# Kernel tuning notes

Measured on AMD Instinct MI355X. Metric: run time of the kernel, lower is better.

The kernel has to match this reference:

```python
import jax, jax.numpy as jnp
import numpy as np

N_NODES = 10000
EPS = 1e-5


def _layernorm(x, gamma, beta):
    mu = jnp.mean(x, axis=-1, keepdims=True)
    var = jnp.mean(jnp.square(x - mu), axis=-1, keepdims=True)
    return (x - mu) * jax.lax.rsqrt(var + EPS) * gamma + beta


def _sage_pool_layer(h, src, dst, Wp, bp, Ws, Wn, b, gamma, beta):
    # DGL SAGEConv(aggregator='pool'):
    #   m_u = relu(h_u @ Wp^T + bp); h_neigh[v] = max_{u in N(v)} m_u (0 if no neighbors)
    #   rst = h @ Ws^T + h_neigh @ Wn^T + b
    m = jax.nn.relu(h @ Wp.T + bp)              # [N, d]
    msg = m[src]                                 # [E, d] gather
    agg = jax.ops.segment_max(msg, dst, num_segments=N_NODES)
    agg = jnp.where(jnp.isfinite(agg), agg, 0.0)  # isolated nodes -> 0
    rst = h @ Ws.T + agg @ Wn.T + b
    # gsage_layer: LayerNorm, then Encoder applies relu (dropout inactive in eval)
    return jax.nn.relu(_layernorm(rst, gamma, beta))


def setup_inputs() -> dict:
    key = jax.random.key(0)
    ks = jax.random.split(key, 16)
    d = 256
    E = 320000
    s = 1.0 / np.sqrt(d)
    inp = {
        "h": jax.random.normal(ks[0], (N_NODES, d), dtype=jnp.float32),
        "edge_src": jax.random.randint(ks[1], (E,), 0, N_NODES, dtype=jnp.int32),
        "edge_dst": jax.random.randint(ks[2], (E,), 0, N_NODES, dtype=jnp.int32),
    }
    for li in range(2):
        kk = jax.random.split(ks[3 + li], 3)
        inp[f"Wp{li}"] = jax.random.normal(kk[0], (d, d), dtype=jnp.float32) * s
        inp[f"bp{li}"] = jnp.zeros((d,), jnp.float32)
        inp[f"Ws{li}"] = jax.random.normal(kk[1], (d, d), dtype=jnp.float32) * s
        inp[f"Wn{li}"] = jax.random.normal(kk[2], (d, d), dtype=jnp.float32) * s
        inp[f"b{li}"] = jnp.zeros((d,), jnp.float32)
        inp[f"g{li}"] = jnp.ones((d,), jnp.float32)
        inp[f"be{li}"] = jnp.zeros((d,), jnp.float32)
    return inp


def reference(h, edge_src, edge_dst,
              Wp0, bp0, Ws0, Wn0, b0, g0, be0,
              Wp1, bp1, Ws1, Wn1, b1, g1, be1):
    h = _sage_pool_layer(h, edge_src, edge_dst, Wp0, bp0, Ws0, Wn0, b0, g0, be0)
    h = _sage_pool_layer(h, edge_src, edge_dst, Wp1, bp1, Ws1, Wn1, b1, g1, be1)
    return h
```

## Files before the change

kernel.cpp:

```cpp
#include <hip/hip_runtime.h>

#define D 256
#define CAP 128
#define ASTRIDE 280
#define LN_EPS 1e-5f

typedef short short8 __attribute__((ext_vector_type(8)));
typedef float floatx4 __attribute__((ext_vector_type(4)));
typedef unsigned short u16x4 __attribute__((ext_vector_type(4)));

typedef const __attribute__((address_space(1))) void* gas_t;
typedef __attribute__((address_space(3))) void* las_t;

#define WAIT_VM(n) __builtin_amdgcn_s_waitcnt(((n) & 0xF) | (((n) >> 4) << 14) | (7 << 4) | (0xF << 8))

__device__ __forceinline__ u16x4 umax4(u16x4 a, u16x4 b) {
#if __has_builtin(__builtin_elementwise_max)
    return __builtin_elementwise_max(a, b);
#else
    u16x4 r;
    r.x = a.x > b.x ? a.x : b.x; r.y = a.y > b.y ? a.y : b.y;
    r.z = a.z > b.z ? a.z : b.z; r.w = a.w > b.w ? a.w : b.w;
    return r;
#endif
}

__device__ __forceinline__ unsigned short f2b(float f) {
    union { float f; unsigned int u; } x; x.f = f;
    unsigned int u = x.u + 0x7FFFu + ((x.u >> 16) & 1u);
    return (unsigned short)(u >> 16);
}

#define GEMM_HALF(APTR_EXPR, WPTR, K0H)                                         \
    {                                                                           \
        short8 aF[4], bF[4][4];                                                 \
        _Pragma("unroll") for (int ks = 0; ks < 4; ks++)                        \
            aF[ks] = APTR_EXPR(K0H + ks * 32);                                  \
        _Pragma("unroll") for (int ks = 0; ks < 4; ks++)                        \
        _Pragma("unroll") for (int t = 0; t < 4; t++)                           \
            bF[ks][t] = *(const short8*)((WPTR) + t * 16 * D + (K0H) + ks * 32);\
        _Pragma("unroll") for (int ks = 0; ks < 4; ks++) {                      \
            acc[0] = __builtin_amdgcn_mfma_f32_16x16x32_bf16(aF[ks], bF[ks][0], acc[0], 0, 0, 0); \
            acc[1] = __builtin_amdgcn_mfma_f32_16x16x32_bf16(aF[ks], bF[ks][1], acc[1], 0, 0, 0); \
            acc[2] = __builtin_amdgcn_mfma_f32_16x16x32_bf16(aF[ks], bF[ks][2], acc[2], 0, 0, 0); \
            acc[3] = __builtin_amdgcn_mfma_f32_16x16x32_bf16(aF[ks], bF[ks][3], acc[3], 0, 0, 0); \
        }                                                                       \
    }

__global__ __launch_bounds__(256) void prep_kernel(
    const float* __restrict__ w0, const float* __restrict__ w1,
    const float* __restrict__ w2, const float* __restrict__ w3,
    const float* __restrict__ w4, const float* __restrict__ w5,
    unsigned short* __restrict__ wb,
    const float* __restrict__ h, unsigned short* __restrict__ hb, int nh4,
    int* __restrict__ cnt, unsigned short* __restrict__ mb, int N)
{
    const int blk = blockIdx.x;
    const int tid = threadIdx.x;
    if (blk < 384) {
        const int wsel = blk >> 6;
        const float* src;
        switch (wsel) {
            case 0: src = w0; break; case 1: src = w1; break;
            case 2: src = w2; break; case 3: src = w3; break;
            case 4: src = w4; break; default: src = w5; break;
        }
        const int idx = (blk & 63) * 1024 + tid * 4;
        const float4 v = *(const float4*)(src + idx);
        ushort4 o;
        o.x = f2b(v.x); o.y = f2b(v.y); o.z = f2b(v.z); o.w = f2b(v.w);
        *(ushort4*)(wb + (size_t)wsel * 65536 + idx) = o;
    } else if (blk < 1024) {
        int i = (blk - 384) * 256 + tid;
        const int stride = 640 * 256;
        for (; i < nh4; i += stride) {
            const float4 v = *(const float4*)(h + (size_t)i * 4);
            ushort4 o;
            o.x = f2b(v.x); o.y = f2b(v.y); o.z = f2b(v.z); o.w = f2b(v.w);
            *(ushort4*)(hb + (size_t)i * 4) = o;
        }
    } else if (blk < 1064) {
        const int i = (blk - 1024) * 256 + tid;
        if (i < N) cnt[i] = 0;
    } else {
        mb[(size_t)N * D + tid] = 0;
    }
}

__global__ __launch_bounds__(64, 4) void gemm_relu(
    const unsigned short* __restrict__ A, const unsigned short* __restrict__ W,
    const float* __restrict__ bias, unsigned short* __restrict__ out_b, int N,
    const int* __restrict__ esrc, const int* __restrict__ edst,
    int* __restrict__ cnt, unsigned short* __restrict__ csr, int E, int ngemm)
{
    if ((int)blockIdx.x >= ngemm) {
        const int nsb = gridDim.x - ngemm;
        int i = ((int)blockIdx.x - ngemm) * 64 + threadIdx.x;
        const int stride = nsb * 64;
        for (; i < E; i += stride) {
            const int d = edst[i];
            const int pos = atomicAdd(&cnt[d], 1);
            if (pos < CAP) csr[(size_t)d * CAP + pos] = (unsigned short)esrc[i];
        }
        return;
    }

    const int lane = threadIdx.x;
    const int quad = lane >> 4;
    const int l16 = lane & 15;
    const int blk = blockIdx.x;
    const int row0 = (blk >> 2) * 16;
    const int col0 = (blk & 3) * 64;
    const int koff = quad * 8;

    floatx4 acc[4];
#pragma unroll
    for (int t = 0; t < 4; t++) acc[t] = (floatx4)(0.f);

    const unsigned short* aptr = A + (size_t)(row0 + l16) * D + koff;
    const unsigned short* wptr = W + (size_t)(col0 + l16) * D + koff;
#define A_GLOBAL(K) (*(const short8*)(aptr + (K)))
    GEMM_HALF(A_GLOBAL, wptr, 0)
    GEMM_HALF(A_GLOBAL, wptr, 128)
#undef A_GLOBAL

#pragma unroll
    for (int t = 0; t < 4; t++) {
        const float bcol = bias[col0 + t * 16 + l16];
#pragma unroll
        for (int r = 0; r < 4; r++) {
            const int rg = row0 + quad * 4 + r;
            const int col = col0 + t * 16 + l16;
            out_b[(size_t)rg * D + col] = f2b(fmaxf(acc[t][r] + bcol, 0.f));
        }
    }
}

__global__ __launch_bounds__(256, 3) void gemm_ln_pool(
    const unsigned short* __restrict__ A, const unsigned short* __restrict__ Wself,
    const unsigned short* __restrict__ Wneigh,
    const unsigned short* __restrict__ mpool,
    const int* __restrict__ cnt, const unsigned short* __restrict__ csr,
    const float* __restrict__ bias,
    const float* __restrict__ gamma, const float* __restrict__ beta,
    unsigned short* __restrict__ out_b, float* __restrict__ out_f,
    const unsigned short* __restrict__ Wnext, const float* __restrict__ bnext,
    unsigned short* __restrict__ mout, int N)
{
    __shared__ unsigned short idxS[16][CAP];
    __shared__ unsigned short gbuf[4][2][8][D];
    __shared__ unsigned short aggS[16 * ASTRIDE];
    __shared__ float redS[4][16], redS2[4][16], muA[16], rsA[16];

    const int tid = threadIdx.x;
    const int wave = tid >> 6;
    const int lane = tid & 63;
    const int quad = lane >> 4;
    const int l16 = lane & 15;
    const int row0 = blockIdx.x * 16;
    const int koff = quad * 8;
    const int rbase = wave * 4;
    const int half = lane >> 5;
    const int l32 = lane & 31;

    int degs[4];
#pragma unroll
    for (int rr = 0; rr < 4; rr++) degs[rr] = min(cnt[row0 + rbase + rr], CAP);
    int P = max(max(degs[0], degs[1]), max(degs[2], degs[3]));
    const int P2 = (P + 1) & ~1;
#pragma unroll
    for (int rr = 0; rr < 4; rr++) {
        const int rg = row0 + rbase + rr;
        for (int i = lane; i < P2; i += 64)
            idxS[rbase + rr][i] = (i < degs[rr]) ? csr[(size_t)rg * CAP + i]
                                                 : (unsigned short)N;
    }

    floatx4 acc[4];
#pragma unroll
    for (int t = 0; t < 4; t++) acc[t] = (floatx4)(0.f);

    {
        const unsigned short* aptr = A + (size_t)(row0 + l16) * D + koff;
        const unsigned short* wptr = Wself + (size_t)(wave * 64 + l16) * D + koff;
#pragma unroll
        for (int k0 = 0; k0 < D; k0 += 32) {
            const short8 av = *(const short8*)(aptr + k0);
            const short8 b0 = *(const short8*)(wptr + k0);
            const short8 b1 = *(const short8*)(wptr + 16 * D + k0);
            const short8 b2 = *(const short8*)(wptr + 32 * D + k0);
            const short8 b3 = *(const short8*)(wptr + 48 * D + k0);
            acc[0] = __builtin_amdgcn_mfma_f32_16x16x32_bf16(av, b0, acc[0], 0, 0, 0);
            acc[1] = __builtin_amdgcn_mfma_f32_16x16x32_bf16(av, b1, acc[1], 0, 0, 0);
            acc[2] = __builtin_amdgcn_mfma_f32_16x16x32_bf16(av, b2, acc[2], 0, 0, 0);
            acc[3] = __builtin_amdgcn_mfma_f32_16x16x32_bf16(av, b3, acc[3], 0, 0, 0);
        }
    }

    {
        const int nb = P2 >> 1;
        u16x4 mx[4];
#pragma unroll
        for (int rr = 0; rr < 4; rr++) mx[rr] = (u16x4)(0);

#define ISSUE_BURST(bi, buf)                                                    \
        {                                                                       \
            _Pragma("unroll") for (int rr = 0; rr < 4; rr++) {                  \
                const int jj = idxS[rbase + rr][2 * (bi) + half];               \
                const unsigned short* gp = mpool + (size_t)jj * D + l32 * 8;    \
                __builtin_amdgcn_global_load_lds(                               \
                    (gas_t)gp, (las_t)&gbuf[wave][buf][rr * 2][0], 16, 0, 0);   \
            }                                                                   \
        }

        if (nb > 0) ISSUE_BURST(0, 0);
        if (nb > 1) ISSUE_BURST(1, 1);
        for (int b = 0; b < nb; b++) {
            if (b + 1 < nb) WAIT_VM(4); else WAIT_VM(0);
            const int buf = b & 1;
#pragma unroll
            for (int rr = 0; rr < 4; rr++) {
                const u16x4 a0 = *(const u16x4*)&gbuf[wave][buf][rr * 2 + 0][lane * 4];
                const u16x4 a1 = *(const u16x4*)&gbuf[wave][buf][rr * 2 + 1][lane * 4];
                mx[rr] = umax4(mx[rr], umax4(a0, a1));
            }
            if (b + 2 < nb) ISSUE_BURST(b + 2, buf);
        }
#undef ISSUE_BURST
#pragma unroll
        for (int rr = 0; rr < 4; rr++)
            *(u16x4*)&aggS[(rbase + rr) * ASTRIDE + lane * 4] = mx[rr];
    }
    __syncthreads();

    {
        const unsigned short* wptr = Wneigh + (size_t)(wave * 64 + l16) * D + koff;
#pragma unroll
        for (int k0 = 0; k0 < D; k0 += 32) {
            const short8 av = *(const short8*)&aggS[l16 * ASTRIDE + koff + k0];
            const short8 b0 = *(const short8*)(wptr + k0);
            const short8 b1 = *(const short8*)(wptr + 16 * D + k0);
            const short8 b2 = *(const short8*)(wptr + 32 * D + k0);
            const short8 b3 = *(const short8*)(wptr + 48 * D + k0);
            acc[0] = __builtin_amdgcn_mfma_f32_16x16x32_bf16(av, b0, acc[0], 0, 0, 0);
            acc[1] = __builtin_amdgcn_mfma_f32_16x16x32_bf16(av, b1, acc[1], 0, 0, 0);
            acc[2] = __builtin_amdgcn_mfma_f32_16x16x32_bf16(av, b2, acc[2], 0, 0, 0);
            acc[3] = __builtin_amdgcn_mfma_f32_16x16x32_bf16(av, b3, acc[3], 0, 0, 0);
        }
    }

    float bcol[4];
#pragma unroll
    for (int t = 0; t < 4; t++) bcol[t] = bias[wave * 64 + t * 16 + l16];
#pragma unroll
    for (int t = 0; t < 4; t++)
#pragma unroll
        for (int r = 0; r < 4; r++) acc[t][r] += bcol[t];

#pragma unroll
    for (int r = 0; r < 4; r++) {
        float s = 0.f, s2 = 0.f;
#pragma unroll
        for (int t = 0; t < 4; t++) {
            const float v = acc[t][r];
            s += v; s2 += v * v;
        }
        s += __shfl_xor(s, 1);  s2 += __shfl_xor(s2, 1);
        s += __shfl_xor(s, 2);  s2 += __shfl_xor(s2, 2);
        s += __shfl_xor(s, 4);  s2 += __shfl_xor(s2, 4);
        s += __shfl_xor(s, 8);  s2 += __shfl_xor(s2, 8);
        if (l16 == 0) {
            redS[wave][quad * 4 + r] = s;
            redS2[wave][quad * 4 + r] = s2;
        }
    }
    __syncthreads();
    if (tid < 16) {
        const float S  = redS[0][tid] + redS[1][tid] + redS[2][tid] + redS[3][tid];
        const float S2 = redS2[0][tid] + redS2[1][tid] + redS2[2][tid] + redS2[3][tid];
        const float mu = S * (1.f / D);
        float var = S2 * (1.f / D) - mu * mu;
        var = fmaxf(var, 0.f);
        muA[tid] = mu;
        rsA[tid] = rsqrtf(var + LN_EPS);
    }
    __syncthreads();

    float gcol[4], becol[4];
#pragma unroll
    for (int t = 0; t < 4; t++) {
        gcol[t] = gamma[wave * 64 + t * 16 + l16];
        becol[t] = beta[wave * 64 + t * 16 + l16];
    }
#pragma unroll
    for (int r = 0; r < 4; r++) {
        const int rl = quad * 4 + r;
        const int rg = row0 + rl;
        const float mu = muA[rl];
        const float rs = rsA[rl];
#pragma unroll
        for (int t = 0; t < 4; t++) {
            const int col = wave * 64 + t * 16 + l16;
            float o = (acc[t][r] - mu) * rs * gcol[t] + becol[t];
            o = fmaxf(o, 0.f);
            const unsigned short ob = f2b(o);
            if (out_f) out_f[(size_t)rg * D + col] = o;
            else       out_b[(size_t)rg * D + col] = ob;
            if (Wnext) aggS[rl * ASTRIDE + col] = ob;
        }
    }

    if (Wnext) {
        __syncthreads();
#pragma unroll
        for (int t = 0; t < 4; t++) acc[t] = (floatx4)(0.f);
        const unsigned short* wptr = Wnext + (size_t)(wave * 64 + l16) * D + koff;
#pragma unroll
        for (int k0 = 0; k0 < D; k0 += 32) {
            const short8 av = *(const short8*)&aggS[l16 * ASTRIDE + koff + k0];
            const short8 b0 = *(const short8*)(wptr + k0);
            const short8 b1 = *(const short8*)(wptr + 16 * D + k0);
            const short8 b2 = *(const short8*)(wptr + 32 * D + k0);
            const short8 b3 = *(const short8*)(wptr + 48 * D + k0);
            acc[0] = __builtin_amdgcn_mfma_f32_16x16x32_bf16(av, b0, acc[0], 0, 0, 0);
            acc[1] = __builtin_amdgcn_mfma_f32_16x16x32_bf16(av, b1, acc[1], 0, 0, 0);
            acc[2] = __builtin_amdgcn_mfma_f32_16x16x32_bf16(av, b2, acc[2], 0, 0, 0);
            acc[3] = __builtin_amdgcn_mfma_f32_16x16x32_bf16(av, b3, acc[3], 0, 0, 0);
        }
#pragma unroll
        for (int t = 0; t < 4; t++) {
            const float bc = bnext[wave * 64 + t * 16 + l16];
#pragma unroll
            for (int r = 0; r < 4; r++) {
                const int rg = row0 + quad * 4 + r;
                const int col = wave * 64 + t * 16 + l16;
                mout[(size_t)rg * D + col] = f2b(fmaxf(acc[t][r] + bc, 0.f));
            }
        }
    }
}

extern "C" void kernel_launch(void* const* d_in, const int* in_sizes, int n_in,
                              void* d_out, int out_size, void* d_ws, size_t ws_size,
                              hipStream_t stream) {
    const float* h    = (const float*)d_in[0];
    const int*   esrc = (const int*)d_in[1];
    const int*   edst = (const int*)d_in[2];
    const float* Wp0  = (const float*)d_in[3];
    const float* bp0  = (const float*)d_in[4];
    const float* Ws0  = (const float*)d_in[5];
    const float* Wn0  = (const float*)d_in[6];
    const float* b0   = (const float*)d_in[7];
    const float* g0   = (const float*)d_in[8];
    const float* be0  = (const float*)d_in[9];
    const float* Wp1  = (const float*)d_in[10];
    const float* bp1  = (const float*)d_in[11];
    const float* Ws1  = (const float*)d_in[12];
    const float* Wn1  = (const float*)d_in[13];
    const float* b1   = (const float*)d_in[14];
    const float* g1   = (const float*)d_in[15];
    const float* be1  = (const float*)d_in[16];

    const int N = in_sizes[0] / D;
    const int E = in_sizes[1];
    const size_t ND = (size_t)N * D;

    unsigned short* hb  = (unsigned short*)d_ws;
    unsigned short* mb  = hb + ND;
    unsigned short* h1b = mb + ND + D;
    unsigned short* wb  = h1b + ND;
    int* cnt = (int*)(wb + 6 * 65536);
    unsigned short* csr = (unsigned short*)(cnt + N);

    unsigned short* wpb0 = wb + 0 * 65536;
    unsigned short* wsb0 = wb + 1 * 65536;
    unsigned short* wnb0 = wb + 2 * 65536;
    unsigned short* wpb1 = wb + 3 * 65536;
    unsigned short* wsb1 = wb + 4 * 65536;
    unsigned short* wnb1 = wb + 5 * 65536;

    const int rblocks = (N / 16) * 4;
    const int pblocks = N / 16;
    const int sblocks = 1024;

    prep_kernel<<<1065, 256, 0, stream>>>(Wp0, Ws0, Wn0, Wp1, Ws1, Wn1, wb,
                                          h, hb, (int)(ND / 4), cnt, mb, N);

    gemm_relu<<<rblocks + sblocks, 64, 0, stream>>>(hb, wpb0, bp0, mb, N,
                                                    esrc, edst, cnt, csr, E, rblocks);
    gemm_ln_pool<<<pblocks, 256, 0, stream>>>(hb, wsb0, wnb0, mb, cnt, csr,
                                              b0, g0, be0, h1b, nullptr,
                                              wpb1, bp1, mb, N);

    gemm_ln_pool<<<pblocks, 256, 0, stream>>>(h1b, wsb1, wnb1, mb, cnt, csr,
                                              b1, g1, be1, nullptr, (float*)d_out,
                                              nullptr, nullptr, nullptr, N);
}
```

Baseline: 215.9 us.

## Gather pooled neighbors into registers with 4-deep prefetch overlapping self GEMM

Replaces the global_load_lds double-buffered neighbor gather with direct 16-byte register loads, issued four batches ahead. The first batches are issued before the self-weight GEMM so gather latency overlaps the MFMA work. Each half-wave covers alternate neighbors, and the two halves are combined with a cross-lane shuffle max. A separate m1b buffer is added so layer 0 writes the next layer's pooled messages without clobbering the mb buffer that other blocks are still reading; this costs extra workspace and higher register pressure from the 16 in-flight vectors.

```diff
diff --git a/kernel.cpp b/kernel.cpp
--- a/kernel.cpp
+++ b/kernel.cpp
@@ -7,20 +7,15 @@
 
 typedef short short8 __attribute__((ext_vector_type(8)));
 typedef float floatx4 __attribute__((ext_vector_type(4)));
-typedef unsigned short u16x4 __attribute__((ext_vector_type(4)));
-
-typedef const __attribute__((address_space(1))) void* gas_t;
-typedef __attribute__((address_space(3))) void* las_t;
-
-#define WAIT_VM(n) __builtin_amdgcn_s_waitcnt(((n) & 0xF) | (((n) >> 4) << 14) | (7 << 4) | (0xF << 8))
-
-__device__ __forceinline__ u16x4 umax4(u16x4 a, u16x4 b) {
+typedef unsigned short u16x8 __attribute__((ext_vector_type(8)));
+
+__device__ __forceinline__ u16x8 umax8(u16x8 a, u16x8 b) {
 #if __has_builtin(__builtin_elementwise_max)
     return __builtin_elementwise_max(a, b);
 #else
-    u16x4 r;
-    r.x = a.x > b.x ? a.x : b.x; r.y = a.y > b.y ? a.y : b.y;
-    r.z = a.z > b.z ? a.z : b.z; r.w = a.w > b.w ? a.w : b.w;
+    u16x8 r;
+#pragma unroll
+    for (int i = 0; i < 8; i++) r[i] = a[i] > b[i] ? a[i] : b[i];
     return r;
 #endif
 }
@@ -53,7 +48,8 @@
     const float* __restrict__ w4, const float* __restrict__ w5,
     unsigned short* __restrict__ wb,
     const float* __restrict__ h, unsigned short* __restrict__ hb, int nh4,
-    int* __restrict__ cnt, unsigned short* __restrict__ mb, int N)
+    int* __restrict__ cnt, unsigned short* __restrict__ mb,
+    unsigned short* __restrict__ m1b, int N)
 {
     const int blk = blockIdx.x;
     const int tid = threadIdx.x;
@@ -84,6 +80,7 @@
         if (i < N) cnt[i] = 0;
     } else {
         mb[(size_t)N * D + tid] = 0;
+        m1b[(size_t)N * D + tid] = 0;
     }
 }
 
@@ -148,7 +145,6 @@
     unsigned short* __restrict__ mout, int N)
 {
     __shared__ unsigned short idxS[16][CAP];
-    __shared__ unsigned short gbuf[4][2][8][D];
     __shared__ unsigned short aggS[16 * ASTRIDE];
     __shared__ float redS[4][16], redS2[4][16], muA[16], rsA[16];
 
@@ -167,13 +163,38 @@
 #pragma unroll
     for (int rr = 0; rr < 4; rr++) degs[rr] = min(cnt[row0 + rbase + rr], CAP);
     int P = max(max(degs[0], degs[1]), max(degs[2], degs[3]));
-    const int P2 = (P + 1) & ~1;
+    const int P2R = (P + 7) & ~7;
 #pragma unroll
     for (int rr = 0; rr < 4; rr++) {
         const int rg = row0 + rbase + rr;
-        for (int i = lane; i < P2; i += 64)
+        for (int i = lane; i < P2R; i += 64)
             idxS[rbase + rr][i] = (i < degs[rr]) ? csr[(size_t)rg * CAP + i]
                                                  : (unsigned short)N;
+    }
+
+    const int nb = P2R >> 1;
+    const unsigned short* mbase = mpool + l32 * 8;
+
+#define ISSUE_B(SL, bi)                                                         \
+    {                                                                           \
+        _Pragma("unroll") for (int rr = 0; rr < 4; rr++) {                      \
+            const int jj = idxS[rbase + rr][2 * (bi) + half];                   \
+            SL[rr] = *(const u16x8*)(mbase + (size_t)jj * D);                   \
+        }                                                                       \
+    }
+#define CONS_B(SL)                                                              \
+    {                                                                           \
+        _Pragma("unroll") for (int rr = 0; rr < 4; rr++)                        \
+            mx[rr] = umax8(mx[rr], SL[rr]);                                     \
+    }
+
+    u16x8 g0[4], g1[4], g2[4], g3[4];
+    u16x8 mx[4];
+#pragma unroll
+    for (int rr = 0; rr < 4; rr++) mx[rr] = (u16x8)(0);
+
+    if (nb) {
+        ISSUE_B(g0, 0) ISSUE_B(g1, 1) ISSUE_B(g2, 2) ISSUE_B(g3, 3)
     }
 
     floatx4 acc[4];
@@ -197,39 +218,25 @@
         }
     }
 
-    {
-        const int nb = P2 >> 1;
-        u16x4 mx[4];
-#pragma unroll
-        for (int rr = 0; rr < 4; rr++) mx[rr] = (u16x4)(0);
-
-#define ISSUE_BURST(bi, buf)                                                    \
-        {                                                                       \
-            _Pragma("unroll") for (int rr = 0; rr < 4; rr++) {                  \
-                const int jj = idxS[rbase + rr][2 * (bi) + half];               \
-                const unsigned short* gp = mpool + (size_t)jj * D + l32 * 8;    \
-                __builtin_amdgcn_global_load_lds(                               \
-                    (gas_t)gp, (las_t)&gbuf[wave][buf][rr * 2][0], 16, 0, 0);   \
-            }                                                                   \
-        }
-
-        if (nb > 0) ISSUE_BURST(0, 0);
-        if (nb > 1) ISSUE_BURST(1, 1);
-        for (int b = 0; b < nb; b++) {
-            if (b + 1 < nb) WAIT_VM(4); else WAIT_VM(0);
-            const int buf = b & 1;
-#pragma unroll
-            for (int rr = 0; rr < 4; rr++) {
-                const u16x4 a0 = *(const u16x4*)&gbuf[wave][buf][rr * 2 + 0][lane * 4];
-                const u16x4 a1 = *(const u16x4*)&gbuf[wave][buf][rr * 2 + 1][lane * 4];
-                mx[rr] = umax4(mx[rr], umax4(a0, a1));
-            }
-            if (b + 2 < nb) ISSUE_BURST(b + 2, buf);
-        }
-#undef ISSUE_BURST
-#pragma unroll
-        for (int rr = 0; rr < 4; rr++)
-            *(u16x4*)&aggS[(rbase + rr) * ASTRIDE + lane * 4] = mx[rr];
+    for (int b = 0; b < nb; b += 4) {
+        const bool more = (b + 8 <= nb);
+        CONS_B(g0) if (more) ISSUE_B(g0, b + 4)
+        CONS_B(g1) if (more) ISSUE_B(g1, b + 5)
+        CONS_B(g2) if (more) ISSUE_B(g2, b + 6)
+        CONS_B(g3) if (more) ISSUE_B(g3, b + 7)
+    }
+#undef ISSUE_B
+#undef CONS_B
+
+#pragma unroll
+    for (int rr = 0; rr < 4; rr++) {
+        union { u16x8 v; int w[4]; } cur, oth;
+        cur.v = mx[rr];
+#pragma unroll
+        for (int k = 0; k < 4; k++) oth.w[k] = __shfl_xor(cur.w[k], 32);
+        const u16x8 mf = umax8(cur.v, oth.v);
+        if (half == 0)
+            *(u16x8*)&aggS[(rbase + rr) * ASTRIDE + l32 * 8] = mf;
     }
     __syncthreads();
 
@@ -371,6 +378,7 @@
     unsigned short* wb  = h1b + ND;
     int* cnt = (int*)(wb + 6 * 65536);
     unsigned short* csr = (unsigned short*)(cnt + N);
+    unsigned short* m1b = csr + (size_t)N * CAP;
 
     unsigned short* wpb0 = wb + 0 * 65536;
     unsigned short* wsb0 = wb + 1 * 65536;
@@ -384,15 +392,15 @@
     const int sblocks = 1024;
 
     prep_kernel<<<1065, 256, 0, stream>>>(Wp0, Ws0, Wn0, Wp1, Ws1, Wn1, wb,
-                                          h, hb, (int)(ND / 4), cnt, mb, N);
+                                          h, hb, (int)(ND / 4), cnt, mb, m1b, N);
 
     gemm_relu<<<rblocks + sblocks, 64, 0, stream>>>(hb, wpb0, bp0, mb, N,
                                                     esrc, edst, cnt, csr, E, rblocks);
     gemm_ln_pool<<<pblocks, 256, 0, stream>>>(hb, wsb0, wnb0, mb, cnt, csr,
                                               b0, g0, be0, h1b, nullptr,
-                                              wpb1, bp1, mb, N);
-
-    gemm_ln_pool<<<pblocks, 256, 0, stream>>>(h1b, wsb1, wnb1, mb, cnt, csr,
+                                              wpb1, bp1, m1b, N);
+
+    gemm_ln_pool<<<pblocks, 256, 0, stream>>>(h1b, wsb1, wnb1, m1b, cnt, csr,
                                               b1, g1, be1, nullptr, (float*)d_out,
                                               nullptr, nullptr, nullptr, N);
 }
```

Measured after the change: 216.5 us. Within noise of the previous version (+0.3%).
